# Kernel optimization log

Hardware: AMD Instinct MI355X
Metric: run time of the kernel (lower is better)

Reference implementation:

```python
import jax, jax.numpy as jnp
import numpy as np

NEG_SLOPE = 0.2

def gat_conv(x, W, att_src, att_dst, src, dst, num_nodes, concat):
    # x: [N, F_in], W: [F_in, H*C], att_*: [H, C]
    H, C = att_src.shape
    h = (x @ W).reshape(-1, H, C)                      # [N, H, C]
    a_src = jnp.sum(h * att_src[None], axis=-1)        # [N, H]
    a_dst = jnp.sum(h * att_dst[None], axis=-1)        # [N, H]
    # per-edge raw attention: alpha_j (source) + alpha_i (target)
    alpha = a_src[src] + a_dst[dst]                    # [E, H]
    alpha = jax.nn.leaky_relu(alpha, NEG_SLOPE)
    # segment softmax over incoming edges of each destination node
    amax = jax.ops.segment_max(alpha, dst, num_segments=num_nodes)  # [N, H]
    amax = jnp.where(jnp.isfinite(amax), amax, 0.0)
    ex = jnp.exp(alpha - amax[dst])                    # [E, H]
    denom = jax.ops.segment_sum(ex, dst, num_segments=num_nodes)    # [N, H]
    attn = ex / (denom[dst] + 1e-16)                   # [E, H]
    # attention-weighted scatter-add aggregation
    msg = h[src] * attn[..., None]                     # [E, H, C]
    out = jax.ops.segment_sum(msg, dst, num_segments=num_nodes)     # [N, H, C]
    if concat:
        return out.reshape(num_nodes, H * C)
    return out.mean(axis=1)


def setup_inputs() -> dict:
    key = jax.random.key(0)
    ks = jax.random.split(key, 8)
    N, E = 100000, 1600000
    F_in, Hid, Hd, F_out = 256, 32, 8, 64
    glorot = lambda k, shape: jax.random.uniform(
        k, shape, jnp.float32, -1.0, 1.0) * jnp.sqrt(6.0 / (shape[0] + shape[-1]))
    x = jax.random.normal(ks[0], (N, F_in), jnp.float32)
    edge_index = jax.random.randint(ks[1], (2, E), 0, N, jnp.int64)
    W1 = glorot(ks[2], (F_in, Hd * Hid))
    att_src1 = glorot(ks[3], (Hd, Hid))
    att_dst1 = glorot(ks[4], (Hd, Hid))
    W2 = glorot(ks[5], (Hd * Hid, 1 * F_out))
    att_src2 = glorot(ks[6], (1, F_out))
    att_dst2 = glorot(ks[7], (1, F_out))
    return {"x": x, "W1": W1, "att_src1": att_src1, "att_dst1": att_dst1,
            "W2": W2, "att_src2": att_src2, "att_dst2": att_dst2,
            "edge_index": edge_index}


def reference(x, W1, att_src1, att_dst1, W2, att_src2, att_dst2, edge_index):
    src, dst = edge_index[0], edge_index[1]
    N = x.shape[0]
    # dropout is inactive in eval mode
    h = gat_conv(x, W1, att_src1, att_dst1, src, dst, N, concat=True)
    h = jax.nn.elu(h)
    out = gat_conv(h, W2, att_src2, att_dst2, src, dst, N, concat=False)
    return out
```

## Files before the change

kernel.cpp:

```cpp
#include <hip/hip_runtime.h>
#include <hip/hip_bf16.h>

#define LRELU(a) ((a) >= 0.0f ? (a) : 0.2f * (a))

typedef __attribute__((ext_vector_type(8))) _Float16 f16x8;
typedef __attribute__((ext_vector_type(4))) _Float16 f16x4;
typedef __attribute__((ext_vector_type(4))) float f32x4;

__global__ __launch_bounds__(256) void cvt_w_t(const float* __restrict__ W,
                                               _Float16* __restrict__ T,
                                               int K, int Nc) {
    int t = blockIdx.x * 256 + threadIdx.x;
    if (t >= K * Nc) return;
    int k = t / Nc, n = t % Nc;
    T[n * K + k] = (_Float16)W[t];
}

__global__ __launch_bounds__(512) void gemm1_mfma(
    const float* __restrict__ A,
    const _Float16* __restrict__ BT,
    const float* __restrict__ attS, const float* __restrict__ attD,
    _Float16* __restrict__ C, float* __restrict__ a_src, float* __restrict__ a_dst,
    int M) {
    const int K = 256;
    __shared__ _Float16 sA[128][40];
    __shared__ _Float16 sB[256][40];
    int tid = threadIdx.x;
    int m0 = blockIdx.y * 128;
    int wid = tid >> 6, lane = tid & 63;
    int wm = (wid >> 2) * 64, wn = (wid & 3) * 64;
    int lr = lane & 15, lg = lane >> 4;

    f32x4 acc[4][4];
    #pragma unroll
    for (int i = 0; i < 4; ++i)
        #pragma unroll
        for (int j = 0; j < 4; ++j)
            acc[i][j] = (f32x4){0.f, 0.f, 0.f, 0.f};

    for (int k0 = 0; k0 < K; k0 += 32) {
        {
            int row = tid >> 2, seg = tid & 3;
            int grow = m0 + row;
            float4 v0 = make_float4(0.f, 0.f, 0.f, 0.f), v1 = v0;
            if (grow < M) {
                v0 = *(const float4*)&A[(size_t)grow * K + k0 + seg * 8];
                v1 = *(const float4*)&A[(size_t)grow * K + k0 + seg * 8 + 4];
            }
            f16x8 hv;
            hv[0] = (_Float16)v0.x; hv[1] = (_Float16)v0.y;
            hv[2] = (_Float16)v0.z; hv[3] = (_Float16)v0.w;
            hv[4] = (_Float16)v1.x; hv[5] = (_Float16)v1.y;
            hv[6] = (_Float16)v1.z; hv[7] = (_Float16)v1.w;
            *(f16x8*)&sA[row][seg * 8] = hv;
        }
        #pragma unroll
        for (int rnd = 0; rnd < 2; ++rnd) {
            int idx = tid + rnd * 512;
            int row = idx >> 2, seg = idx & 3;
            *(f16x8*)&sB[row][seg * 8] = *(const f16x8*)&BT[(size_t)row * K + k0 + seg * 8];
        }
        __syncthreads();
        f16x8 bfr[4];
        #pragma unroll
        for (int i = 0; i < 4; ++i)
            bfr[i] = *(const f16x8*)&sB[wn + i * 16 + lr][lg * 8];
        #pragma unroll
        for (int mi = 0; mi < 4; ++mi) {
            f16x8 av = *(const f16x8*)&sA[wm + mi * 16 + lr][lg * 8];
            #pragma unroll
            for (int ni = 0; ni < 4; ++ni)
                acc[mi][ni] = __builtin_amdgcn_mfma_f32_16x16x32_f16(av, bfr[ni], acc[mi][ni], 0, 0, 0);
        }
        __syncthreads();
    }

    float asv[4], adv[4];
    #pragma unroll
    for (int ni = 0; ni < 4; ++ni) {
        int col = wn + ni * 16 + lr;
        asv[ni] = attS[col];
        adv[ni] = attD[col];
    }
    int head0 = wn >> 5;
    #pragma unroll
    for (int mi = 0; mi < 4; ++mi) {
        #pragma unroll
        for (int r = 0; r < 4; ++r) {
            int row = m0 + wm + mi * 16 + lg * 4 + r;
            float v0 = acc[mi][0][r], v1 = acc[mi][1][r];
            float v2 = acc[mi][2][r], v3 = acc[mi][3][r];
            float ps0 = v0 * asv[0] + v1 * asv[1], pd0 = v0 * adv[0] + v1 * adv[1];
            float ps1 = v2 * asv[2] + v3 * asv[3], pd1 = v2 * adv[2] + v3 * adv[3];
            #pragma unroll
            for (int msk = 8; msk >= 1; msk >>= 1) {
                ps0 += __shfl_xor(ps0, msk); pd0 += __shfl_xor(pd0, msk);
                ps1 += __shfl_xor(ps1, msk); pd1 += __shfl_xor(pd1, msk);
            }
            if (row < M) {
                C[(size_t)row * 256 + wn +  0 + lr] = (_Float16)v0;
                C[(size_t)row * 256 + wn + 16 + lr] = (_Float16)v1;
                C[(size_t)row * 256 + wn + 32 + lr] = (_Float16)v2;
                C[(size_t)row * 256 + wn + 48 + lr] = (_Float16)v3;
                if (lr == 0) {
                    a_src[(size_t)row * 8 + head0]     = ps0;
                    a_dst[(size_t)row * 8 + head0]     = pd0;
                    a_src[(size_t)row * 8 + head0 + 1] = ps1;
                    a_dst[(size_t)row * 8 + head0 + 1] = pd1;
                }
            }
        }
    }
}

__global__ __launch_bounds__(256) void gemm2_mfma(
    const _Float16* __restrict__ A,
    const _Float16* __restrict__ BT,
    const float* __restrict__ attS, const float* __restrict__ attD,
    _Float16* __restrict__ C, float* __restrict__ a_src, float* __restrict__ a_dst,
    int M) {
    const int K = 256;
    __shared__ _Float16 sA[128][40];
    __shared__ _Float16 sB[64][40];
    int tid = threadIdx.x;
    int m0 = blockIdx.y * 128;
    int wid = tid >> 6, lane = tid & 63;
    int wm = wid * 32;
    int lr = lane & 15, lg = lane >> 4;

    f32x4 acc[2][4];
    #pragma unroll
    for (int i = 0; i < 2; ++i)
        #pragma unroll
        for (int j = 0; j < 4; ++j)
            acc[i][j] = (f32x4){0.f, 0.f, 0.f, 0.f};

    for (int k0 = 0; k0 < K; k0 += 32) {
        #pragma unroll
        for (int rnd = 0; rnd < 2; ++rnd) {
            int idx = tid + rnd * 256;
            int row = idx >> 2, seg = idx & 3;
            int grow = m0 + row;
            f16x8 va = {0, 0, 0, 0, 0, 0, 0, 0};
            if (grow < M) va = *(const f16x8*)&A[(size_t)grow * K + k0 + seg * 8];
            *(f16x8*)&sA[row][seg * 8] = va;
        }
        {
            int row = tid >> 2, seg = tid & 3;
            *(f16x8*)&sB[row][seg * 8] = *(const f16x8*)&BT[(size_t)row * K + k0 + seg * 8];
        }
        __syncthreads();
        f16x8 bfr[4];
        #pragma unroll
        for (int i = 0; i < 4; ++i)
            bfr[i] = *(const f16x8*)&sB[i * 16 + lr][lg * 8];
        #pragma unroll
        for (int mi = 0; mi < 2; ++mi) {
            f16x8 av = *(const f16x8*)&sA[wm + mi * 16 + lr][lg * 8];
            #pragma unroll
            for (int ni = 0; ni < 4; ++ni)
                acc[mi][ni] = __builtin_amdgcn_mfma_f32_16x16x32_f16(av, bfr[ni], acc[mi][ni], 0, 0, 0);
        }
        __syncthreads();
    }

    float asv[4], adv[4];
    #pragma unroll
    for (int ni = 0; ni < 4; ++ni) {
        asv[ni] = attS[ni * 16 + lr];
        adv[ni] = attD[ni * 16 + lr];
    }
    #pragma unroll
    for (int mi = 0; mi < 2; ++mi) {
        #pragma unroll
        for (int r = 0; r < 4; ++r) {
            int row = m0 + wm + mi * 16 + lg * 4 + r;
            float ps = 0.f, pd = 0.f;
            #pragma unroll
            for (int ni = 0; ni < 4; ++ni) {
                float v = acc[mi][ni][r];
                ps += v * asv[ni];
                pd += v * adv[ni];
            }
            #pragma unroll
            for (int msk = 8; msk >= 1; msk >>= 1) {
                ps += __shfl_xor(ps, msk);
                pd += __shfl_xor(pd, msk);
            }
            if (row < M) {
                #pragma unroll
                for (int ni = 0; ni < 4; ++ni)
                    C[(size_t)row * 64 + ni * 16 + lr] = (_Float16)acc[mi][ni][r];
                if (lr == 0) { a_src[row] = ps; a_dst[row] = pd; }
            }
        }
    }
}

__global__ __launch_bounds__(256) void hist_dst(const int* __restrict__ dst, unsigned* __restrict__ cnt, int E) {
    int e = blockIdx.x * 256 + threadIdx.x;
    if (e < E) atomicAdd(&cnt[dst[e]], 1u);
}

__global__ __launch_bounds__(256) void scan_partial(const unsigned* __restrict__ cnt,
                                                    int* __restrict__ rowptr,
                                                    unsigned* __restrict__ bsum, int n) {
    __shared__ unsigned s[256];
    int i = blockIdx.x * 256 + threadIdx.x;
    unsigned v = (i < n) ? cnt[i] : 0u;
    s[threadIdx.x] = v;
    __syncthreads();
    #pragma unroll
    for (int off = 1; off < 256; off <<= 1) {
        unsigned t = (threadIdx.x >= off) ? s[threadIdx.x - off] : 0u;
        __syncthreads();
        s[threadIdx.x] += t;
        __syncthreads();
    }
    if (i < n) rowptr[i + 1] = (int)s[threadIdx.x];
    if (threadIdx.x == 255) bsum[blockIdx.x] = s[255];
}

__global__ __launch_bounds__(512) void scan_bsum(unsigned* __restrict__ bsum, int nb) {
    __shared__ unsigned s[512];
    int t = threadIdx.x;
    s[t] = (t < nb) ? bsum[t] : 0u;
    __syncthreads();
    #pragma unroll
    for (int off = 1; off < 512; off <<= 1) {
        unsigned v = (t >= off) ? s[t - off] : 0u;
        __syncthreads();
        s[t] += v;
        __syncthreads();
    }
    unsigned ex = (t == 0) ? 0u : s[t - 1];
    if (t < nb) bsum[t] = ex;
}

__global__ __launch_bounds__(256) void scan_add(int* __restrict__ rowptr, const unsigned* __restrict__ boff, int n) {
    int i = blockIdx.x * 256 + threadIdx.x;
    if (i < n) rowptr[i + 1] += (int)boff[blockIdx.x];
    if (blockIdx.x == 0 && threadIdx.x == 0) rowptr[0] = 0;
}

__global__ __launch_bounds__(256) void scatter_srcs(const int* __restrict__ src, const int* __restrict__ dst,
                                                    const int* __restrict__ rowptr,
                                                    unsigned* __restrict__ cnt, int* __restrict__ srcs, int E) {
    int e = blockIdx.x * 256 + threadIdx.x;
    if (e >= E) return;
    int d = dst[e];
    unsigned p = atomicAdd(&cnt[d], 1u);
    srcs[rowptr[d] + (int)p] = src[e];
}

__global__ __launch_bounds__(256) void agg1(const int* __restrict__ srcs,
                                            const int* __restrict__ rowptr,
                                            const float* __restrict__ a_src,
                                            const float* __restrict__ a_dst,
                                            const _Float16* __restrict__ h1,
                                            _Float16* __restrict__ o1, int N) {
    int wid = threadIdx.x >> 6;
    int lane = threadIdx.x & 63;
    int d = blockIdx.x * 4 + wid;
    if (d >= N) return;
    int beg = rowptr[d], end = rowptr[d + 1];
    int e8 = lane & 7;
    int hd = lane >> 3;
    float adst = a_dst[(size_t)d * 8 + hd];
    const char* h1b = (const char*)h1;
    const char* asb = (const char*)a_src;
    unsigned loff = (unsigned)(lane << 3);

    float4 acc = make_float4(0.f, 0.f, 0.f, 0.f);
    float wsum = 0.0f;
    for (int j0 = beg; j0 < end; j0 += 8) {
        int nb = end - j0; if (nb > 8) nb = 8;
        int s2 = 0; float w = 0.f;
        if (e8 < nb) {
            s2 = srcs[j0 + e8];
            float a = *(const float*)(asb + (((unsigned)s2 << 5) + ((unsigned)hd << 2))) + adst;
            a = LRELU(a);
            w = __expf(a);
        }
        wsum += w;
        #pragma unroll 8
        for (int t = 0; t < 8; ++t) {
            if (t >= nb) break;
            int sl = (lane & 56) | t;
            float at = __shfl(w, sl);
            int s = __shfl(s2, sl);
            f16x4 hq = *(const f16x4*)(h1b + (((unsigned)s << 9) + loff));
            acc.x += (float)hq[0] * at;
            acc.y += (float)hq[1] * at;
            acc.z += (float)hq[2] * at;
            acc.w += (float)hq[3] * at;
        }
    }
    wsum += __shfl_xor(wsum, 1);
    wsum += __shfl_xor(wsum, 2);
    wsum += __shfl_xor(wsum, 4);
    float rw = 1.0f / (wsum + 1e-16f);
    acc.x *= rw; acc.y *= rw; acc.z *= rw; acc.w *= rw;
    acc.x = acc.x > 0.0f ? acc.x : expm1f(acc.x);
    acc.y = acc.y > 0.0f ? acc.y : expm1f(acc.y);
    acc.z = acc.z > 0.0f ? acc.z : expm1f(acc.z);
    acc.w = acc.w > 0.0f ? acc.w : expm1f(acc.w);
    f16x4 hh;
    hh[0] = (_Float16)acc.x;
    hh[1] = (_Float16)acc.y;
    hh[2] = (_Float16)acc.z;
    hh[3] = (_Float16)acc.w;
    *(f16x4*)(o1 + (size_t)d * 256 + lane * 4) = hh;
}

__global__ __launch_bounds__(256) void agg2(const int* __restrict__ srcs,
                                            const int* __restrict__ rowptr,
                                            const float* __restrict__ a_src,
                                            const float* __restrict__ a_dst,
                                            const _Float16* __restrict__ h2,
                                            float* __restrict__ out, int N) {
    int wid = threadIdx.x >> 6;
    int lane = threadIdx.x & 63;
    int d = blockIdx.x * 4 + wid;
    if (d >= N) return;
    int beg = rowptr[d], end = rowptr[d + 1];
    float adst = a_dst[d];
    const char* h2b = (const char*)h2;
    int grp = lane >> 4;
    int cid = lane & 15;

    float4 acc = make_float4(0.f, 0.f, 0.f, 0.f);
    float wsum = 0.0f;
    for (int j0 = beg; j0 < end; j0 += 64) {
        int nb = end - j0; if (nb > 64) nb = 64;
        int s2 = 0; float w = 0.f;
        if (lane < nb) {
            s2 = srcs[j0 + lane];
            float a = LRELU(a_src[s2] + adst);
            w = __expf(a);
        }
        wsum += w;
        int tmax = (nb + 3) >> 2;
        for (int t = 0; t < tmax; ++t) {
            int ei = 4 * t + grp;
            float at = __shfl(w, ei);
            int s = __shfl(s2, ei);
            f16x4 hv = *(const f16x4*)(h2b + (((unsigned)s << 7) + ((unsigned)cid << 3)));
            acc.x += (float)hv[0] * at;
            acc.y += (float)hv[1] * at;
            acc.z += (float)hv[2] * at;
            acc.w += (float)hv[3] * at;
        }
    }
    #pragma unroll
    for (int mask = 16; mask <= 32; mask <<= 1) {
        acc.x += __shfl_xor(acc.x, mask);
        acc.y += __shfl_xor(acc.y, mask);
        acc.z += __shfl_xor(acc.z, mask);
        acc.w += __shfl_xor(acc.w, mask);
    }
    #pragma unroll
    for (int mask = 1; mask < 64; mask <<= 1)
        wsum += __shfl_xor(wsum, mask);
    float rw = 1.0f / (wsum + 1e-16f);
    if (lane < 16) {
        float4 o = make_float4(acc.x * rw, acc.y * rw, acc.z * rw, acc.w * rw);
        *(float4*)(out + (size_t)d * 64 + cid * 4) = o;
    }
}

extern "C" void kernel_launch(void* const* d_in, const int* in_sizes, int n_in,
                              void* d_out, int out_size, void* d_ws, size_t ws_size,
                              hipStream_t stream) {
    const float* x        = (const float*)d_in[0];
    const float* W1       = (const float*)d_in[1];
    const float* att_src1 = (const float*)d_in[2];
    const float* att_dst1 = (const float*)d_in[3];
    const float* W2       = (const float*)d_in[4];
    const float* att_src2 = (const float*)d_in[5];
    const float* att_dst2 = (const float*)d_in[6];
    const int*   ei       = (const int*)d_in[7];

    int N = in_sizes[0] / 256;
    int E = in_sizes[7] / 2;
    const int* src = ei;
    const int* dst = ei + E;

    _Float16* out1 = (_Float16*)d_ws;
    _Float16* h1f  = out1 + (size_t)N * 256;
    float* a_src1v = (float*)(h1f + (size_t)N * 256);
    float* a_dst1v = a_src1v + (size_t)N * 8;
    float* a_src2v = a_dst1v + (size_t)N * 8;
    float* a_dst2v = a_src2v + N;
    int*   rowptr  = (int*)(a_dst2v + N);
    unsigned* cnt  = (unsigned*)(rowptr + N + 1);
    int*   srcs    = (int*)(cnt + N);
    unsigned* bsum = (unsigned*)(srcs + E);
    _Float16* w1t  = (_Float16*)(bsum + 512);
    _Float16* w2t  = w1t + 65536;

    _Float16* h2f = h1f;

    float* outf = (float*)d_out;
    int nb = (N + 255) / 256;

    hipMemsetAsync(cnt, 0, (size_t)N * sizeof(unsigned), stream);
    hist_dst<<<(E + 255) / 256, 256, 0, stream>>>(dst, cnt, E);
    scan_partial<<<nb, 256, 0, stream>>>(cnt, rowptr, bsum, N);
    scan_bsum<<<1, 512, 0, stream>>>(bsum, nb);
    scan_add<<<nb, 256, 0, stream>>>(rowptr, bsum, N);
    hipMemsetAsync(cnt, 0, (size_t)N * sizeof(unsigned), stream);
    scatter_srcs<<<(E + 255) / 256, 256, 0, stream>>>(src, dst, rowptr, cnt, srcs, E);

    cvt_w_t<<<(65536 + 255) / 256, 256, 0, stream>>>(W1, w1t, 256, 256);
    cvt_w_t<<<(16384 + 255) / 256, 256, 0, stream>>>(W2, w2t, 256, 64);

    gemm1_mfma<<<dim3(1, (N + 127) / 128), 512, 0, stream>>>(x, w1t,
                                                             att_src1, att_dst1,
                                                             h1f, a_src1v, a_dst1v, N);
    agg1<<<(N + 3) / 4, 256, 0, stream>>>(srcs, rowptr, a_src1v, a_dst1v, h1f, out1, N);

    gemm2_mfma<<<dim3(1, (N + 127) / 128), 256, 0, stream>>>(out1, w2t,
                                                             att_src2, att_dst2,
                                                             h2f, a_src2v, a_dst2v, N);
    agg2<<<(N + 3) / 4, 256, 0, stream>>>(srcs, rowptr, a_src2v, a_dst2v, h2f, outf, N);
}
```

Measured before the change: 486.3 us.

## Replace 3-kernel scan with atomic wave-offset assignment and batch agg1 gathers

Builds the CSR segments without a global prefix scan. Each wave does a shuffle scan over its counts and reserves a base offset with one atomic, giving per-node begin and cursor arrays. scatter_srcs then atomically advances the cursor, and the final cursor serves as the segment end. This drops two kernel launches and one memset, but segments are no longer in node order. Separately, agg1's inner loop now issues all eight gather loads before the FMAs when a full batch of eight edges is present, to raise memory-level parallelism.

After: 493.4 us. No clear change (+1.5%).

```diff
diff --git a/kernel.cpp b/kernel.cpp
--- a/kernel.cpp
+++ b/kernel.cpp
@@ -202,59 +202,37 @@
     if (e < E) atomicAdd(&cnt[dst[e]], 1u);
 }
 
-__global__ __launch_bounds__(256) void scan_partial(const unsigned* __restrict__ cnt,
-                                                    int* __restrict__ rowptr,
-                                                    unsigned* __restrict__ bsum, int n) {
-    __shared__ unsigned s[256];
+__global__ __launch_bounds__(256) void assign_off(const unsigned* __restrict__ cnt,
+                                                  int* __restrict__ begA,
+                                                  int* __restrict__ curB,
+                                                  unsigned* __restrict__ gctr, int n) {
     int i = blockIdx.x * 256 + threadIdx.x;
-    unsigned v = (i < n) ? cnt[i] : 0u;
-    s[threadIdx.x] = v;
-    __syncthreads();
-    #pragma unroll
-    for (int off = 1; off < 256; off <<= 1) {
-        unsigned t = (threadIdx.x >= off) ? s[threadIdx.x - off] : 0u;
-        __syncthreads();
-        s[threadIdx.x] += t;
-        __syncthreads();
-    }
-    if (i < n) rowptr[i + 1] = (int)s[threadIdx.x];
-    if (threadIdx.x == 255) bsum[blockIdx.x] = s[255];
-}
-
-__global__ __launch_bounds__(512) void scan_bsum(unsigned* __restrict__ bsum, int nb) {
-    __shared__ unsigned s[512];
-    int t = threadIdx.x;
-    s[t] = (t < nb) ? bsum[t] : 0u;
-    __syncthreads();
-    #pragma unroll
-    for (int off = 1; off < 512; off <<= 1) {
-        unsigned v = (t >= off) ? s[t - off] : 0u;
-        __syncthreads();
-        s[t] += v;
-        __syncthreads();
-    }
-    unsigned ex = (t == 0) ? 0u : s[t - 1];
-    if (t < nb) bsum[t] = ex;
-}
-
-__global__ __launch_bounds__(256) void scan_add(int* __restrict__ rowptr, const unsigned* __restrict__ boff, int n) {
-    int i = blockIdx.x * 256 + threadIdx.x;
-    if (i < n) rowptr[i + 1] += (int)boff[blockIdx.x];
-    if (blockIdx.x == 0 && threadIdx.x == 0) rowptr[0] = 0;
+    int lane = threadIdx.x & 63;
+    unsigned c = (i < n) ? cnt[i] : 0u;
+    unsigned x = c;
+    #pragma unroll
+    for (int off = 1; off < 64; off <<= 1) {
+        unsigned y = __shfl_up(x, off);
+        if (lane >= off) x += y;
+    }
+    unsigned base = 0;
+    if (lane == 63) base = atomicAdd(gctr, x);
+    base = __shfl(base, 63);
+    unsigned beg = base + x - c;
+    if (i < n) { begA[i] = (int)beg; curB[i] = (int)beg; }
 }
 
 __global__ __launch_bounds__(256) void scatter_srcs(const int* __restrict__ src, const int* __restrict__ dst,
-                                                    const int* __restrict__ rowptr,
-                                                    unsigned* __restrict__ cnt, int* __restrict__ srcs, int E) {
+                                                    int* __restrict__ curB, int* __restrict__ srcs, int E) {
     int e = blockIdx.x * 256 + threadIdx.x;
     if (e >= E) return;
-    int d = dst[e];
-    unsigned p = atomicAdd(&cnt[d], 1u);
-    srcs[rowptr[d] + (int)p] = src[e];
+    int p = atomicAdd(&curB[dst[e]], 1);
+    srcs[p] = src[e];
 }
 
 __global__ __launch_bounds__(256) void agg1(const int* __restrict__ srcs,
-                                            const int* __restrict__ rowptr,
+                                            const int* __restrict__ begA,
+                                            const int* __restrict__ endB,
                                             const float* __restrict__ a_src,
                                             const float* __restrict__ a_dst,
                                             const _Float16* __restrict__ h1,
@@ -263,7 +241,7 @@
     int lane = threadIdx.x & 63;
     int d = blockIdx.x * 4 + wid;
     if (d >= N) return;
-    int beg = rowptr[d], end = rowptr[d + 1];
+    int beg = begA[d], end = endB[d];
     int e8 = lane & 7;
     int hd = lane >> 3;
     float adst = a_dst[(size_t)d * 8 + hd];
@@ -274,7 +252,7 @@
     float4 acc = make_float4(0.f, 0.f, 0.f, 0.f);
     float wsum = 0.0f;
     for (int j0 = beg; j0 < end; j0 += 8) {
-        int nb = end - j0; if (nb > 8) nb = 8;
+        int nb = end - j0;
         int s2 = 0; float w = 0.f;
         if (e8 < nb) {
             s2 = srcs[j0 + e8];
@@ -283,17 +261,36 @@
             w = __expf(a);
         }
         wsum += w;
-        #pragma unroll 8
-        for (int t = 0; t < 8; ++t) {
-            if (t >= nb) break;
-            int sl = (lane & 56) | t;
-            float at = __shfl(w, sl);
-            int s = __shfl(s2, sl);
-            f16x4 hq = *(const f16x4*)(h1b + (((unsigned)s << 9) + loff));
-            acc.x += (float)hq[0] * at;
-            acc.y += (float)hq[1] * at;
-            acc.z += (float)hq[2] * at;
-            acc.w += (float)hq[3] * at;
+        if (nb >= 8) {
+            float at[8]; unsigned sb[8];
+            #pragma unroll
+            for (int t = 0; t < 8; ++t) {
+                int sl = (lane & 56) | t;
+                at[t] = __shfl(w, sl);
+                sb[t] = ((unsigned)__shfl(s2, sl)) << 9;
+            }
+            f16x4 hv[8];
+            #pragma unroll
+            for (int t = 0; t < 8; ++t)
+                hv[t] = *(const f16x4*)(h1b + (sb[t] + loff));
+            #pragma unroll
+            for (int t = 0; t < 8; ++t) {
+                acc.x += (float)hv[t][0] * at[t];
+                acc.y += (float)hv[t][1] * at[t];
+                acc.z += (float)hv[t][2] * at[t];
+                acc.w += (float)hv[t][3] * at[t];
+            }
+        } else {
+            for (int t = 0; t < nb; ++t) {
+                int sl = (lane & 56) | t;
+                float at = __shfl(w, sl);
+                int s = __shfl(s2, sl);
+                f16x4 hq = *(const f16x4*)(h1b + (((unsigned)s << 9) + loff));
+                acc.x += (float)hq[0] * at;
+                acc.y += (float)hq[1] * at;
+                acc.z += (float)hq[2] * at;
+                acc.w += (float)hq[3] * at;
+            }
         }
     }
     wsum += __shfl_xor(wsum, 1);
@@ -314,7 +311,8 @@
 }
 
 __global__ __launch_bounds__(256) void agg2(const int* __restrict__ srcs,
-                                            const int* __restrict__ rowptr,
+                                            const int* __restrict__ begA,
+                                            const int* __restrict__ endB,
                                             const float* __restrict__ a_src,
                                             const float* __restrict__ a_dst,
                                             const _Float16* __restrict__ h2,
@@ -323,7 +321,7 @@
     int lane = threadIdx.x & 63;
     int d = blockIdx.x * 4 + wid;
     if (d >= N) return;
-    int beg = rowptr[d], end = rowptr[d + 1];
+    int beg = begA[d], end = endB[d];
     float adst = a_dst[d];
     const char* h2b = (const char*)h2;
     int grp = lane >> 4;
@@ -392,11 +390,12 @@
     float* a_dst1v = a_src1v + (size_t)N * 8;
     float* a_src2v = a_dst1v + (size_t)N * 8;
     float* a_dst2v = a_src2v + N;
-    int*   rowptr  = (int*)(a_dst2v + N);
-    unsigned* cnt  = (unsigned*)(rowptr + N + 1);
-    int*   srcs    = (int*)(cnt + N);
-    unsigned* bsum = (unsigned*)(srcs + E);
-    _Float16* w1t  = (_Float16*)(bsum + 512);
+    int*   begA    = (int*)(a_dst2v + N);
+    int*   curB    = begA + N;
+    unsigned* cnt  = (unsigned*)(curB + N);
+    unsigned* gctr = cnt + N;
+    int*   srcs    = (int*)(gctr + 1);
+    _Float16* w1t  = (_Float16*)(srcs + E);
     _Float16* w2t  = w1t + 65536;
 
     _Float16* h2f = h1f;
@@ -404,13 +403,10 @@
     float* outf = (float*)d_out;
     int nb = (N + 255) / 256;
 
-    hipMemsetAsync(cnt, 0, (size_t)N * sizeof(unsigned), stream);
+    hipMemsetAsync(cnt, 0, ((size_t)N + 1) * sizeof(unsigned), stream);
     hist_dst<<<(E + 255) / 256, 256, 0, stream>>>(dst, cnt, E);
-    scan_partial<<<nb, 256, 0, stream>>>(cnt, rowptr, bsum, N);
-    scan_bsum<<<1, 512, 0, stream>>>(bsum, nb);
-    scan_add<<<nb, 256, 0, stream>>>(rowptr, bsum, N);
-    hipMemsetAsync(cnt, 0, (size_t)N * sizeof(unsigned), stream);
-    scatter_srcs<<<(E + 255) / 256, 256, 0, stream>>>(src, dst, rowptr, cnt, srcs, E);
+    assign_off<<<nb, 256, 0, stream>>>(cnt, begA, curB, gctr, N);
+    scatter_srcs<<<(E + 255) / 256, 256, 0, stream>>>(src, dst, curB, srcs, E);
 
     cvt_w_t<<<(65536 + 255) / 256, 256, 0, stream>>>(W1, w1t, 256, 256);
     cvt_w_t<<<(16384 + 255) / 256, 256, 0, stream>>>(W2, w2t, 256, 64);
@@ -418,10 +414,10 @@
     gemm1_mfma<<<dim3(1, (N + 127) / 128), 512, 0, stream>>>(x, w1t,
                                                              att_src1, att_dst1,
                                                              h1f, a_src1v, a_dst1v, N);
-    agg1<<<(N + 3) / 4, 256, 0, stream>>>(srcs, rowptr, a_src1v, a_dst1v, h1f, out1, N);
+    agg1<<<(N + 3) / 4, 256, 0, stream>>>(srcs, begA, curB, a_src1v, a_dst1v, h1f, out1, N);
 
     gemm2_mfma<<<dim3(1, (N + 127) / 128), 256, 0, stream>>>(out1, w2t,
                                                              att_src2, att_dst2,
                                                              h2f, a_src2v, a_dst2v, N);
-    agg2<<<(N + 3) / 4, 256, 0, stream>>>(srcs, rowptr, a_src2v, a_dst2v, h2f, outf, N);
-}
+    agg2<<<(N + 3) / 4, 256, 0, stream>>>(srcs, begA, curB, a_src2v, a_dst2v, h2f, outf, N);
+}
```
